# Optimization experiments

Measured on AMD Instinct MI355X. Metric: run time of the kernel, lower is better.

The kernel has to match this reference:

```python
import jax, jax.numpy as jnp
import numpy as np

B, T, V, F = 32, 128, 128, 64
K_ORDER = 3
N_FILT = 64

def setup_inputs() -> dict:
    key = jax.random.key(0)
    k1, k2, k3 = jax.random.split(key, 3)
    x = jax.random.normal(k1, (B, T, V, F), dtype=jnp.float32)
    W = jax.random.uniform(k2, (B, V, V), dtype=jnp.float32)  # learned adjacency, nonneg
    # keras 'uniform' initializer default range [-0.05, 0.05]
    Theta = jax.random.uniform(k3, (K_ORDER, F, N_FILT), dtype=jnp.float32, minval=-0.05, maxval=0.05)
    return {"x": x, "W": W, "Theta": Theta}

def reference(x, W, Theta):
    # x: (B,T,V,F), W: (B,V,V), Theta: (k,F,O)
    k = Theta.shape[0]
    v = x.shape[2]
    eye = jnp.eye(v, dtype=x.dtype)
    deg = jnp.sum(W, axis=1)                      # (B,V) -- sum over axis=1 as in K.sum(W, axis=1)
    D = eye[None, :, :] * deg[:, :, None]         # matrix_diag(deg)
    L = D - W
    L_t = L - eye[None, :, :]                     # 2*L/lambda_max - I with lambda_max=2
    chebs = [jnp.broadcast_to(eye[None, :, :], W.shape), L_t]
    for i in range(2, k):
        # NOTE: elementwise multiply, faithful to the original tf code (tf `*`)
        chebs.append(2.0 * L_t * chebs[-1] - chebs[-2])
    Tk = jnp.stack(chebs, axis=0)                 # (k,B,V,V)
    # out[b,t,u,o] = sum_{k,v,f} Tk[k,b,v,u] * x[b,t,v,f] * Theta[k,f,o]
    # (T_k transposed matmul graph_signal, then dot with theta_k, summed over k and t-batched)
    out = jnp.einsum('kbvu,btvf,kfo->btuo', Tk, x, Theta)
    return jax.nn.relu(out)
```

## Files before the change

### kernel.cpp

```cpp
#include <hip/hip_runtime.h>

typedef __attribute__((ext_vector_type(8))) short bf16x8;
typedef __attribute__((ext_vector_type(4))) float f32x4;

namespace {

constexpr int B = 32, T = 128, V = 128, F = 64, O = 64;
constexpr int TPB = 16;

constexpr size_t WS_THT_OFF = (size_t)B * 64 * 64 * 8 * 2;
constexpr size_t WS_LDG_OFF = WS_THT_OFF + 1536 * 8 * 2;

__device__ inline unsigned short f2bf(float f) {
    unsigned u = __builtin_bit_cast(unsigned, f);
    u += 0x7FFFu + ((u >> 16) & 1u);
    return (unsigned short)(u >> 16);
}

__global__ __launch_bounds__(256) void prep(const float* __restrict__ W,
                                            const float* __restrict__ Theta,
                                            unsigned short* __restrict__ acat_f,
                                            unsigned short* __restrict__ tht_f,
                                            float* __restrict__ ldg) {
    const int tid = threadIdx.x;
    if (blockIdx.x == B) {
        for (int i = 0; i < 6; ++i) {
            int fi = tid + i * 256;
            int ks = fi / 768, rem = fi % 768;
            int nf = rem >> 6, lane = rem & 63;
            int n = nf * 16 + (lane & 15);
            int f0 = ks * 32 + (lane >> 4) * 8;
            unsigned short vals[8];
#pragma unroll
            for (int j = 0; j < 8; ++j) {
                int f = f0 + j;
                float v;
                if (n < 64)       v = Theta[f * 64 + n] - Theta[2 * 4096 + f * 64 + n];
                else if (n < 128) v = Theta[4096 + f * 64 + (n - 64)];
                else              v = Theta[2 * 4096 + f * 64 + (n - 128)];
                vals[j] = f2bf(v);
            }
            *(bf16x8*)(tht_f + (size_t)fi * 8) = *(bf16x8*)vals;
        }
        return;
    }
    const int b = blockIdx.x;
    const float* Wb = W + (size_t)b * V * V;
    __shared__ float Wl[V][V + 1];
    for (int i = 0; i < V * V / 256; ++i) {
        int idx = tid + i * 256;
        Wl[idx >> 7][idx & 127] = Wb[idx];
    }
    __syncthreads();
    if (tid < V) {
        float s = 0.f;
        for (int i = 0; i < V; ++i) s += Wl[i][tid];
        ldg[b * V + tid] = s - 1.0f - Wl[tid][tid];
    }
    unsigned short* ab_f = acat_f + (size_t)b * 32768;
    for (int i = 0; i < 16; ++i) {
        int fi = tid + i * 256;
        int ks = fi >> 9, rem = fi & 511;
        int r2 = rem >> 6, lane = rem & 63;
        int u = r2 * 16 + (lane & 15);
        int kv0 = ks * 32 + (lane >> 4) * 8;
        unsigned short vals[8];
#pragma unroll
        for (int j = 0; j < 8; ++j) {
            int kv = kv0 + j, v = kv & 127;
            float wv = Wl[v][u];
            float val = (v == u) ? 0.f : ((kv < 128) ? -wv : 2.f * wv * wv);
            vals[j] = f2bf(val);
        }
        *(bf16x8*)(ab_f + (size_t)fi * 8) = *(bf16x8*)vals;
    }
}

__global__ __launch_bounds__(512, 1) void graph_conv_main(
    const float* __restrict__ x, const unsigned short* __restrict__ acat_f,
    const unsigned short* __restrict__ tht_f, const float* __restrict__ ldg,
    float* __restrict__ out) {
    const int t0 = blockIdx.x * TPB, b = blockIdx.y;
    const int tid = threadIdx.x;
    const int lane = tid & 63, w = tid >> 6;
    const int uq = w & 3;
    const int oh = w >> 2;
    const int lr = lane & 15, lg = lane >> 4;

    __shared__ __align__(16) float xbuf[2][V * F];
    __shared__ __align__(16) unsigned short zc1[8192];
    __shared__ __align__(16) unsigned short zc2[8192];

    const float* xb = x + ((size_t)(b * T + t0)) * (V * F);

    bf16x8 af_r[2][8];
#pragma unroll
    for (int ks = 0; ks < 8; ++ks)
#pragma unroll
        for (int uf = 0; uf < 2; ++uf)
            af_r[uf][ks] = *(const bf16x8*)(acat_f +
                (((size_t)b * 64 + ks * 8 + 2 * uq + uf) * 64 + lane) * 8);

    bf16x8 th_r[3][2][2];
#pragma unroll
    for (int m = 0; m < 3; ++m)
#pragma unroll
        for (int i = 0; i < 2; ++i)
#pragma unroll
            for (int kf = 0; kf < 2; ++kf) {
                int nf = m * 4 + 2 * oh + i;
                th_r[m][i][kf] = *(const bf16x8*)(tht_f + ((size_t)(kf * 12 + nf) * 64 + lane) * 8);
            }

    f32x4 ldv[2], ld2v[2];
#pragma unroll
    for (int uf = 0; uf < 2; ++uf) {
        ldv[uf] = *(const f32x4*)(ldg + b * V + 32 * uq + 16 * uf + lg * 4);
        ld2v[uf] = 2.0f * ldv[uf] * ldv[uf];
    }

    auto stage_x = [&](int tt, int buf) {
        const char* src = (const char*)(xb + (size_t)tt * (V * F));
        char* dst = (char*)&xbuf[buf][0] + w * 4096;
#pragma unroll
        for (int j = 0; j < 4; ++j) {
            int n = j * 64 + lane;
            int rloc = n >> 4, slot = n & 15;
            int e = ((rloc & 3) << 1) | ((rloc >> 3) & 1);
            int row = 16 * w + rloc;
            const char* g = src + row * 256 + ((slot ^ e) << 4);
            __builtin_amdgcn_global_load_lds(
                (const __attribute__((address_space(1))) void*)g,
                (__attribute__((address_space(3))) void*)(dst + n * 16), 16, 0, 0);
        }
    };

    stage_x(0, 0);
    asm volatile("s_waitcnt vmcnt(0)" ::: "memory");
    __builtin_amdgcn_sched_barrier(0);
    __builtin_amdgcn_s_barrier();
    __builtin_amdgcn_sched_barrier(0);

    const int eL = ((lr & 3) << 1) | ((lr >> 3) & 1);

    for (int tt = 0; tt < TPB; ++tt) {
        const int cur = tt & 1;

        if (tt + 1 < TPB) {
            stage_x(tt + 1, cur ^ 1);
            asm volatile("s_waitcnt vmcnt(4)" ::: "memory");
        } else {
            asm volatile("s_waitcnt vmcnt(0)" ::: "memory");
        }
        __builtin_amdgcn_sched_barrier(0);
        __builtin_amdgcn_s_barrier();
        __builtin_amdgcn_sched_barrier(0);

        bf16x8 xa[2][2];
        const char* xc = (const char*)&xbuf[cur][0];
#pragma unroll
        for (int rv = 0; rv < 2; ++rv) {
            const char* rp = xc + (32 * uq + 16 * rv + lr) * 256;
#pragma unroll
            for (int kf = 0; kf < 2; ++kf) {
                const int s0 = kf * 8 + lg * 2;
                f32x4 a0 = *(const f32x4*)(rp + ((s0 ^ eL) << 4));
                f32x4 a1 = *(const f32x4*)(rp + (((s0 + 1) ^ eL) << 4));
                uint4 u;
                u.x = f2bf(a0[0]) | ((unsigned)f2bf(a0[1]) << 16);
                u.y = f2bf(a0[2]) | ((unsigned)f2bf(a0[3]) << 16);
                u.z = f2bf(a1[0]) | ((unsigned)f2bf(a1[1]) << 16);
                u.w = f2bf(a1[2]) | ((unsigned)f2bf(a1[3]) << 16);
                xa[rv][kf] = __builtin_bit_cast(bf16x8, u);
            }
        }

        f32x4 acc[2][2], z1[2][2], z2[2][2];
#pragma unroll
        for (int a = 0; a < 2; ++a)
#pragma unroll
            for (int o = 0; o < 2; ++o) {
                acc[a][o] = (f32x4){0.f, 0.f, 0.f, 0.f};
                z1[a][o] = (f32x4){0.f, 0.f, 0.f, 0.f};
                z2[a][o] = (f32x4){0.f, 0.f, 0.f, 0.f};
            }
#pragma unroll
        for (int kf = 0; kf < 2; ++kf)
#pragma unroll
            for (int rv = 0; rv < 2; ++rv)
#pragma unroll
                for (int i = 0; i < 2; ++i) {
                    acc[rv][i] = __builtin_amdgcn_mfma_f32_16x16x32_bf16(xa[rv][kf], th_r[0][i][kf], acc[rv][i], 0, 0, 0);
                    z1[rv][i] = __builtin_amdgcn_mfma_f32_16x16x32_bf16(xa[rv][kf], th_r[1][i][kf], z1[rv][i], 0, 0, 0);
                    z2[rv][i] = __builtin_amdgcn_mfma_f32_16x16x32_bf16(xa[rv][kf], th_r[2][i][kf], z2[rv][i], 0, 0, 0);
                }

#pragma unroll
        for (int uf = 0; uf < 2; ++uf)
#pragma unroll
            for (int of = 0; of < 2; ++of) {
                acc[uf][of] += ldv[uf] * z1[uf][of] + ld2v[uf] * z2[uf][of];
                const int ro = 32 * oh + of * 16 + lr;
                const int slot = 4 * uq + 2 * uf + (lg >> 1);
                const int byte = ro * 256 + (((slot ^ eL)) << 4) + (lg & 1) * 8;
                f32x4 v1 = z1[uf][of], v2 = z2[uf][of];
                uint2 q1, q2;
                q1.x = f2bf(v1[0]) | ((unsigned)f2bf(v1[1]) << 16);
                q1.y = f2bf(v1[2]) | ((unsigned)f2bf(v1[3]) << 16);
                q2.x = f2bf(v2[0]) | ((unsigned)f2bf(v2[1]) << 16);
                q2.y = f2bf(v2[2]) | ((unsigned)f2bf(v2[3]) << 16);
                *(uint2*)((char*)zc1 + byte) = q1;
                *(uint2*)((char*)zc2 + byte) = q2;
            }

        asm volatile("s_waitcnt lgkmcnt(0)" ::: "memory");
        __builtin_amdgcn_sched_barrier(0);
        __builtin_amdgcn_s_barrier();
        __builtin_amdgcn_sched_barrier(0);

#pragma unroll
        for (int kk = 0; kk < 8; ++kk) {
            const char* zsrc = (kk < 4) ? (const char*)zc1 : (const char*)zc2;
            bf16x8 zb[2];
#pragma unroll
            for (int of = 0; of < 2; ++of) {
                const int ro = 32 * oh + of * 16 + lr;
                const int slot = (kk & 3) * 4 + lg;
                zb[of] = *(const bf16x8*)(zsrc + ro * 256 + ((slot ^ eL) << 4));
            }
#pragma unroll
            for (int uf = 0; uf < 2; ++uf)
#pragma unroll
                for (int of = 0; of < 2; ++of)
                    acc[uf][of] = __builtin_amdgcn_mfma_f32_16x16x32_bf16(af_r[uf][kk], zb[of], acc[uf][of], 0, 0, 0);
        }

        float* obt = out + ((size_t)(b * T + t0 + tt)) * (V * O);
#pragma unroll
        for (int uf = 0; uf < 2; ++uf)
#pragma unroll
            for (int of = 0; of < 2; ++of)
#pragma unroll
                for (int j = 0; j < 4; ++j) {
                    const int u = 32 * uq + 16 * uf + lg * 4 + j;
                    const int o = 32 * oh + 16 * of + lr;
                    const float r = acc[uf][of][j];
                    obt[u * 64 + o] = r > 0.f ? r : 0.f;
                }
    }
}

}

extern "C" void kernel_launch(void* const* d_in, const int* in_sizes, int n_in,
                              void* d_out, int out_size, void* d_ws, size_t ws_size,
                              hipStream_t stream) {
    const float* x = (const float*)d_in[0];
    const float* W = (const float*)d_in[1];
    const float* Theta = (const float*)d_in[2];
    float* outp = (float*)d_out;

    unsigned short* acat_f = (unsigned short*)d_ws;
    unsigned short* tht_f = (unsigned short*)((char*)d_ws + WS_THT_OFF);
    float* ldg = (float*)((char*)d_ws + WS_LDG_OFF);

    prep<<<B + 1, 256, 0, stream>>>(W, Theta, acat_f, tht_f, ldg);
    graph_conv_main<<<dim3(T / TPB, B), 512, 0, stream>>>(x, acat_f, tht_f, ldg, outp);
}
```

Baseline: 92.34 us.

## Stage operands in LDS, prefetch x via registers as bf16, coalesce output stores

Moves the adjacency and Theta fragments from registers into shared memory, freeing VGPRs. x is now prefetched two timesteps ahead into registers and converted to bf16 once before being written to LDS, where the old code read fp32 and converted on every read. Output tiles are staged through LDS and written as coalesced float4 stores instead of scattered scalar stores. The cost is more barriers per timestep, extra LDS traffic for the A and Theta fragments, and heavier LDS usage.

```diff
diff --git a/kernel.cpp b/kernel.cpp
--- a/kernel.cpp
+++ b/kernel.cpp
@@ -87,30 +87,12 @@
     const int oh = w >> 2;
     const int lr = lane & 15, lg = lane >> 4;
 
-    __shared__ __align__(16) float xbuf[2][V * F];
-    __shared__ __align__(16) unsigned short zc1[8192];
-    __shared__ __align__(16) unsigned short zc2[8192];
+    __shared__ __align__(16) unsigned short tht_s[12288];
+    __shared__ __align__(16) unsigned short acat_s[32768];
+    __shared__ __align__(16) unsigned short xbuf[2][8192];
+    __shared__ __align__(16) unsigned short zc[16384];
 
     const float* xb = x + ((size_t)(b * T + t0)) * (V * F);
-
-    bf16x8 af_r[2][8];
-#pragma unroll
-    for (int ks = 0; ks < 8; ++ks)
-#pragma unroll
-        for (int uf = 0; uf < 2; ++uf)
-            af_r[uf][ks] = *(const bf16x8*)(acat_f +
-                (((size_t)b * 64 + ks * 8 + 2 * uq + uf) * 64 + lane) * 8);
-
-    bf16x8 th_r[3][2][2];
-#pragma unroll
-    for (int m = 0; m < 3; ++m)
-#pragma unroll
-        for (int i = 0; i < 2; ++i)
-#pragma unroll
-            for (int kf = 0; kf < 2; ++kf) {
-                int nf = m * 4 + 2 * oh + i;
-                th_r[m][i][kf] = *(const bf16x8*)(tht_f + ((size_t)(kf * 12 + nf) * 64 + lane) * 8);
-            }
 
     f32x4 ldv[2], ld2v[2];
 #pragma unroll
@@ -119,60 +101,66 @@
         ld2v[uf] = 2.0f * ldv[uf] * ldv[uf];
     }
 
-    auto stage_x = [&](int tt, int buf) {
-        const char* src = (const char*)(xb + (size_t)tt * (V * F));
-        char* dst = (char*)&xbuf[buf][0] + w * 4096;
-#pragma unroll
-        for (int j = 0; j < 4; ++j) {
-            int n = j * 64 + lane;
-            int rloc = n >> 4, slot = n & 15;
-            int e = ((rloc & 3) << 1) | ((rloc >> 3) & 1);
-            int row = 16 * w + rloc;
-            const char* g = src + row * 256 + ((slot ^ e) << 4);
+    {
+        const unsigned short* ag = acat_f + (size_t)b * 32768;
+#pragma unroll
+        for (int i = 0; i < 8; ++i) {
+            int c = tid + i * 512;
             __builtin_amdgcn_global_load_lds(
-                (const __attribute__((address_space(1))) void*)g,
-                (__attribute__((address_space(3))) void*)(dst + n * 16), 16, 0, 0);
-        }
+                (const __attribute__((address_space(1))) void*)(ag + c * 8),
+                (__attribute__((address_space(3))) void*)(acat_s + c * 8), 16, 0, 0);
+        }
+#pragma unroll
+        for (int i = 0; i < 3; ++i) {
+            int c = tid + i * 512;
+            __builtin_amdgcn_global_load_lds(
+                (const __attribute__((address_space(1))) void*)(tht_f + c * 8),
+                (__attribute__((address_space(3))) void*)(tht_s + c * 8), 16, 0, 0);
+        }
+    }
+
+    auto load_pf = [&](int tt, float4 (&pf)[4]) {
+        const float4* src = (const float4*)(xb + (size_t)tt * (V * F));
+#pragma unroll
+        for (int i = 0; i < 4; ++i) pf[i] = src[tid + i * 512];
     };
-
-    stage_x(0, 0);
+    auto store_pf = [&](int buf, float4 (&pf)[4]) {
+#pragma unroll
+        for (int i = 0; i < 4; ++i) {
+            int p = tid + i * 512;
+            int row = p >> 4, c4 = p & 15;
+            uint2 q;
+            q.x = f2bf(pf[i].x) | ((unsigned)f2bf(pf[i].y) << 16);
+            q.y = f2bf(pf[i].z) | ((unsigned)f2bf(pf[i].w) << 16);
+            *(uint2*)((char*)xbuf[buf] +
+                      row * 128 + (((c4 >> 1) ^ (row & 7)) << 4) + (c4 & 1) * 8) = q;
+        }
+    };
+
+    float4 pfA[4], pfB[4];
+    load_pf(0, pfA);
+    load_pf(1, pfB);
     asm volatile("s_waitcnt vmcnt(0)" ::: "memory");
+    __builtin_amdgcn_sched_barrier(0);
+    store_pf(0, pfA);
+    asm volatile("s_waitcnt lgkmcnt(0)" ::: "memory");
     __builtin_amdgcn_sched_barrier(0);
     __builtin_amdgcn_s_barrier();
     __builtin_amdgcn_sched_barrier(0);
 
-    const int eL = ((lr & 3) << 1) | ((lr >> 3) & 1);
-
-    for (int tt = 0; tt < TPB; ++tt) {
+    auto iter = [&](int tt, float4 (&pfRdy)[4], float4 (&pfNew)[4]) {
         const int cur = tt & 1;
-
-        if (tt + 1 < TPB) {
-            stage_x(tt + 1, cur ^ 1);
-            asm volatile("s_waitcnt vmcnt(4)" ::: "memory");
-        } else {
-            asm volatile("s_waitcnt vmcnt(0)" ::: "memory");
-        }
-        __builtin_amdgcn_sched_barrier(0);
-        __builtin_amdgcn_s_barrier();
-        __builtin_amdgcn_sched_barrier(0);
+        if (tt + 2 < TPB) load_pf(tt + 2, pfNew);
 
         bf16x8 xa[2][2];
-        const char* xc = (const char*)&xbuf[cur][0];
 #pragma unroll
         for (int rv = 0; rv < 2; ++rv) {
-            const char* rp = xc + (32 * uq + 16 * rv + lr) * 256;
-#pragma unroll
-            for (int kf = 0; kf < 2; ++kf) {
-                const int s0 = kf * 8 + lg * 2;
-                f32x4 a0 = *(const f32x4*)(rp + ((s0 ^ eL) << 4));
-                f32x4 a1 = *(const f32x4*)(rp + (((s0 + 1) ^ eL) << 4));
-                uint4 u;
-                u.x = f2bf(a0[0]) | ((unsigned)f2bf(a0[1]) << 16);
-                u.y = f2bf(a0[2]) | ((unsigned)f2bf(a0[3]) << 16);
-                u.z = f2bf(a1[0]) | ((unsigned)f2bf(a1[1]) << 16);
-                u.w = f2bf(a1[2]) | ((unsigned)f2bf(a1[3]) << 16);
-                xa[rv][kf] = __builtin_bit_cast(bf16x8, u);
-            }
+            const int row = 32 * uq + 16 * rv + lr;
+            const char* rp = (const char*)xbuf[cur] + row * 128;
+            const int rs = row & 7;
+#pragma unroll
+            for (int kf = 0; kf < 2; ++kf)
+                xa[rv][kf] = *(const bf16x8*)(rp + (((kf * 4 + lg) ^ rs) << 4));
         }
 
         f32x4 acc[2][2], z1[2][2], z2[2][2];
@@ -187,14 +175,20 @@
 #pragma unroll
         for (int kf = 0; kf < 2; ++kf)
 #pragma unroll
-            for (int rv = 0; rv < 2; ++rv)
-#pragma unroll
-                for (int i = 0; i < 2; ++i) {
-                    acc[rv][i] = __builtin_amdgcn_mfma_f32_16x16x32_bf16(xa[rv][kf], th_r[0][i][kf], acc[rv][i], 0, 0, 0);
-                    z1[rv][i] = __builtin_amdgcn_mfma_f32_16x16x32_bf16(xa[rv][kf], th_r[1][i][kf], z1[rv][i], 0, 0, 0);
-                    z2[rv][i] = __builtin_amdgcn_mfma_f32_16x16x32_bf16(xa[rv][kf], th_r[2][i][kf], z2[rv][i], 0, 0, 0);
+            for (int i = 0; i < 2; ++i) {
+                bf16x8 t0b = *(const bf16x8*)(tht_s + ((kf * 12 + 0 + 2 * oh + i) * 64 + lane) * 8);
+                bf16x8 t1b = *(const bf16x8*)(tht_s + ((kf * 12 + 4 + 2 * oh + i) * 64 + lane) * 8);
+                bf16x8 t2b = *(const bf16x8*)(tht_s + ((kf * 12 + 8 + 2 * oh + i) * 64 + lane) * 8);
+#pragma unroll
+                for (int rv = 0; rv < 2; ++rv) {
+                    acc[rv][i] = __builtin_amdgcn_mfma_f32_16x16x32_bf16(xa[rv][kf], t0b, acc[rv][i], 0, 0, 0);
+                    z1[rv][i] = __builtin_amdgcn_mfma_f32_16x16x32_bf16(xa[rv][kf], t1b, z1[rv][i], 0, 0, 0);
+                    z2[rv][i] = __builtin_amdgcn_mfma_f32_16x16x32_bf16(xa[rv][kf], t2b, z2[rv][i], 0, 0, 0);
                 }
-
+            }
+
+        char* zc1p = (char*)zc;
+        char* zc2p = (char*)zc + 16384;
 #pragma unroll
         for (int uf = 0; uf < 2; ++uf)
 #pragma unroll
@@ -202,15 +196,15 @@
                 acc[uf][of] += ldv[uf] * z1[uf][of] + ld2v[uf] * z2[uf][of];
                 const int ro = 32 * oh + of * 16 + lr;
                 const int slot = 4 * uq + 2 * uf + (lg >> 1);
-                const int byte = ro * 256 + (((slot ^ eL)) << 4) + (lg & 1) * 8;
+                const int byte = ro * 256 + (((slot ^ lr)) << 4) + (lg & 1) * 8;
                 f32x4 v1 = z1[uf][of], v2 = z2[uf][of];
                 uint2 q1, q2;
                 q1.x = f2bf(v1[0]) | ((unsigned)f2bf(v1[1]) << 16);
                 q1.y = f2bf(v1[2]) | ((unsigned)f2bf(v1[3]) << 16);
                 q2.x = f2bf(v2[0]) | ((unsigned)f2bf(v2[1]) << 16);
                 q2.y = f2bf(v2[2]) | ((unsigned)f2bf(v2[3]) << 16);
-                *(uint2*)((char*)zc1 + byte) = q1;
-                *(uint2*)((char*)zc2 + byte) = q2;
+                *(uint2*)(zc1p + byte) = q1;
+                *(uint2*)(zc2p + byte) = q2;
             }
 
         asm volatile("s_waitcnt lgkmcnt(0)" ::: "memory");
@@ -220,22 +214,41 @@
 
 #pragma unroll
         for (int kk = 0; kk < 8; ++kk) {
-            const char* zsrc = (kk < 4) ? (const char*)zc1 : (const char*)zc2;
+            const char* zsrc = (kk < 4) ? zc1p : zc2p;
+            bf16x8 af[2];
+#pragma unroll
+            for (int uf = 0; uf < 2; ++uf)
+                af[uf] = *(const bf16x8*)(acat_s + ((kk * 8 + 2 * uq + uf) * 64 + lane) * 8);
             bf16x8 zb[2];
 #pragma unroll
             for (int of = 0; of < 2; ++of) {
                 const int ro = 32 * oh + of * 16 + lr;
                 const int slot = (kk & 3) * 4 + lg;
-                zb[of] = *(const bf16x8*)(zsrc + ro * 256 + ((slot ^ eL) << 4));
+                zb[of] = *(const bf16x8*)(zsrc + ro * 256 + ((slot ^ lr) << 4));
             }
 #pragma unroll
             for (int uf = 0; uf < 2; ++uf)
 #pragma unroll
                 for (int of = 0; of < 2; ++of)
-                    acc[uf][of] = __builtin_amdgcn_mfma_f32_16x16x32_bf16(af_r[uf][kk], zb[of], acc[uf][of], 0, 0, 0);
-        }
-
-        float* obt = out + ((size_t)(b * T + t0 + tt)) * (V * O);
+                    acc[uf][of] = __builtin_amdgcn_mfma_f32_16x16x32_bf16(af[uf], zb[of], acc[uf][of], 0, 0, 0);
+        }
+
+        if (tt + 1 < TPB) {
+            if (tt + 2 < TPB) {
+                asm volatile("s_waitcnt vmcnt(4)" ::: "memory");
+            } else {
+                asm volatile("s_waitcnt vmcnt(0)" ::: "memory");
+            }
+            __builtin_amdgcn_sched_barrier(0);
+            store_pf(cur ^ 1, pfRdy);
+        }
+
+        asm volatile("s_waitcnt lgkmcnt(0)" ::: "memory");
+        __builtin_amdgcn_sched_barrier(0);
+        __builtin_amdgcn_s_barrier();
+        __builtin_amdgcn_sched_barrier(0);
+
+        float* os = (float*)zc;
 #pragma unroll
         for (int uf = 0; uf < 2; ++uf)
 #pragma unroll
@@ -245,8 +258,33 @@
                     const int u = 32 * uq + 16 * uf + lg * 4 + j;
                     const int o = 32 * oh + 16 * of + lr;
                     const float r = acc[uf][of][j];
-                    obt[u * 64 + o] = r > 0.f ? r : 0.f;
+                    os[u * 64 + o] = r > 0.f ? r : 0.f;
                 }
+
+        asm volatile("s_waitcnt lgkmcnt(0)" ::: "memory");
+        __builtin_amdgcn_sched_barrier(0);
+        __builtin_amdgcn_s_barrier();
+        __builtin_amdgcn_sched_barrier(0);
+
+        {
+            float* obt = out + ((size_t)(b * T + t0 + tt)) * (V * O);
+            const float4* osv = (const float4*)zc;
+#pragma unroll
+            for (int i = 0; i < 4; ++i) {
+                const int idx = tid + i * 512;
+                *(float4*)(obt + idx * 4) = osv[idx];
+            }
+        }
+
+        asm volatile("s_waitcnt lgkmcnt(0)" ::: "memory");
+        __builtin_amdgcn_sched_barrier(0);
+        __builtin_amdgcn_s_barrier();
+        __builtin_amdgcn_sched_barrier(0);
+    };
+
+    for (int tt = 0; tt < TPB; tt += 2) {
+        iter(tt, pfB, pfA);
+        iter(tt + 1, pfA, pfB);
     }
 }
 
```

New measurement: 79.22 us. 14.2% less time.
